# Performance work log

Measured on AMD Instinct MI355X. Metric: run time of the kernel, lower is better.

The kernel has to match this reference:

```python
import jax, jax.numpy as jnp
import numpy as np

B, T, N, F_IN = 8, 16, 1000, 16
E = 16000
H, D = 4, 32          # heads, gat_hidden_shape
HL = 64               # lstm hidden
OUT = 8
NEG_SLOPE = 0.2       # PyG GATConv default


def setup_inputs() -> dict:
    key = jax.random.key(0)
    ks = jax.random.split(key, 10)
    def init(k, shape, fan):
        return (jax.random.normal(k, shape, jnp.float32) / np.sqrt(fan)).astype(jnp.float32)
    x = jax.random.normal(ks[0], (B, T, N, F_IN), jnp.float32)
    edge_index = jax.random.randint(ks[1], (2, E), 0, N)
    W_gat = init(ks[2], (F_IN, H * D), F_IN)       # GATConv lin weight
    att_src = init(ks[3], (H, D), D)
    att_dst = init(ks[4], (H, D), D)
    b_gat = jnp.zeros((H * D,), jnp.float32)
    W_ih = init(ks[5], (4 * HL, H * D), H * D)     # LSTM, gate order i,f,g,o
    W_hh = init(ks[6], (4 * HL, HL), HL)
    b_ih = jnp.zeros((4 * HL,), jnp.float32)
    b_hh = jnp.zeros((4 * HL,), jnp.float32)
    W_clf = init(ks[7], (OUT, HL), HL)
    b_clf = jnp.zeros((OUT,), jnp.float32)
    return {"x": x, "edge_index": edge_index, "W_gat": W_gat, "att_src": att_src,
            "att_dst": att_dst, "b_gat": b_gat, "W_ih": W_ih, "W_hh": W_hh,
            "b_ih": b_ih, "b_hh": b_hh, "W_clf": W_clf, "b_clf": b_clf}


def reference(x, edge_index, W_gat, att_src, att_dst, b_gat,
              W_ih, W_hh, b_ih, b_hh, W_clf, b_clf):
    Bx, Tx, Nx, Fx = x.shape
    x_flat = x.reshape(Bx * Tx, Nx, Fx)
    # PyG GATConv adds self-loops by default
    loop = jnp.arange(Nx)
    src = jnp.concatenate([edge_index[0], loop])
    dst = jnp.concatenate([edge_index[1], loop])

    def gat_graph(xg):  # xg: [N, F]
        xp = (xg @ W_gat).reshape(Nx, H, D)                 # [N,H,D]
        a_s = jnp.einsum('nhd,hd->nh', xp, att_src)         # [N,H]
        a_d = jnp.einsum('nhd,hd->nh', xp, att_dst)
        e = jax.nn.leaky_relu(a_s[src] + a_d[dst], NEG_SLOPE)  # [E+N,H]
        m = jax.ops.segment_max(e, dst, num_segments=Nx)       # per-target softmax
        ex = jnp.exp(e - m[dst])
        denom = jax.ops.segment_sum(ex, dst, num_segments=Nx)
        alpha = ex / denom[dst]                                # [E+N,H]
        out = jax.ops.segment_sum(alpha[..., None] * xp[src], dst, num_segments=Nx)
        return out.reshape(Nx, H * D) + b_gat                  # [N, H*D]

    gat = jax.vmap(gat_graph)(x_flat)          # [B*T, N, H*D]
    gat = jax.nn.relu(gat)
    pooled = gat.max(axis=1)                   # global_max_pool -> [B*T, H*D]
    seq = pooled.reshape(Bx, Tx, H * D)

    h0 = jnp.zeros((Bx, HL), jnp.float32)
    c0 = jnp.zeros((Bx, HL), jnp.float32)

    def step(carry, xt):  # xt: [B, H*D]
        h, c = carry
        gates = xt @ W_ih.T + h @ W_hh.T + b_ih + b_hh
        i, f, g, o = jnp.split(gates, 4, axis=-1)
        i, f, o = jax.nn.sigmoid(i), jax.nn.sigmoid(f), jax.nn.sigmoid(o)
        g = jnp.tanh(g)
        c = f * c + i * g
        h = o * jnp.tanh(c)
        return (h, c), None

    (hT, _), _ = jax.lax.scan(step, (h0, c0), seq.transpose(1, 0, 2))
    return hT @ W_clf.T + b_clf                # [B, OUT]
```

## Files before the change

kernel.cpp:

```cpp
#include <hip/hip_runtime.h>
#include <hip/hip_bf16.h>
#include <stdint.h>

namespace {
constexpr int kB = 8, kT = 16, kN = 1000, kF = 16;
constexpr int kE = 16000;
constexpr int kH = 4, kHD = 128;
constexpr int kHL = 64, kOUT = 8;
constexpr int kG = kB * kT;
constexpr float kNeg = 0.2f;
constexpr int kNB = 25;
constexpr int kNPB = 40;
constexpr int kPre = 1024;
constexpr int kNPW = 32;
constexpr int kBCAP = 64;

constexpr size_t CX_WG   = 0;
constexpr size_t CX_ATS  = CX_WG   + 2048;
constexpr size_t CX_ATD  = CX_ATS  + 128;
constexpr size_t CX_BG   = CX_ATD  + 128;
constexpr size_t CX_WIH  = CX_BG   + 128;
constexpr size_t CX_WHH  = CX_WIH  + 32768;
constexpr size_t CX_BIH  = CX_WHH  + 16384;
constexpr size_t CX_BHH  = CX_BIH  + 256;
constexpr size_t CX_WCLF = CX_BHH  + 256;
constexpr size_t CX_BCLF = CX_WCLF + 512;
constexpr size_t CX_TOTAL = CX_BCLF + 8;

constexpr size_t OFF_FLAG  = 0;
constexpr size_t OFF_ROW   = 256;
constexpr size_t OFF_COL   = 4352;
constexpr size_t OFF_POOL  = 68608;
constexpr size_t OFF_CANON = 134400;
constexpr size_t OFF_AS    = 239872;
constexpr size_t OFF_PPART = OFF_AS + (size_t)kG * 288000;
constexpr size_t PPART_BYTES = (size_t)kG * kNB * kHD * 4;
constexpr size_t OFF_BUCKET = OFF_PPART + PPART_BYTES;
constexpr size_t BUCKET_BYTES = (size_t)kN * kBCAP * 4;

constexpr int kSetupBlocks = 41;
}

typedef float v2f __attribute__((ext_vector_type(2)));

__device__ __forceinline__ float bf2f(unsigned short u) {
    return __uint_as_float(((uint32_t)u) << 16);
}
__device__ __forceinline__ float blo(uint32_t u) { return __uint_as_float(u << 16); }
__device__ __forceinline__ float bhi(uint32_t u) { return __uint_as_float(u & 0xffff0000u); }
__device__ __forceinline__ unsigned short f2bf(float f) {
    uint32_t u = __float_as_uint(f);
    uint32_t r = (u + 0x7fff + ((u >> 16) & 1)) >> 16;
    return (unsigned short)r;
}
__device__ __forceinline__ float sigm(float x) { return 1.f / (1.f + __expf(-x)); }

__device__ __forceinline__ int detect_isf_wave(const unsigned short* xs, int lane) {
    const uint2 s4 = *(const uint2*)(xs + lane * 4);
    const unsigned short u0 = (unsigned short)(s4.x & 0xffff);
    const unsigned short u1 = (unsigned short)(s4.x >> 16);
    const unsigned short u2 = (unsigned short)(s4.y & 0xffff);
    const unsigned short u3 = (unsigned short)(s4.y >> 16);
    int loc = 0;
#define ISF_TEST(u) { int ex = ((u) >> 7) & 0xff; \
    loc += ((u) == 0 || (ex >= 97 && ex <= 143)) ? 1 : 0; }
    ISF_TEST(u0) ISF_TEST(u1) ISF_TEST(u2) ISF_TEST(u3)
#undef ISF_TEST
#pragma unroll
    for (int sft = 1; sft < 64; sft <<= 1) loc += __shfl_xor(loc, sft, 64);
    return (loc >= 205) ? 0 : 1;
}

struct ConvArgs {
    const unsigned short* src[10];
    int n[10];
};

__global__ __launch_bounds__(256) void mega_setup(
        const void* __restrict__ xraw, const int* __restrict__ ei,
        ConvArgs ca,
        const unsigned short* __restrict__ WgR,
        const unsigned short* __restrict__ atsR,
        const unsigned short* __restrict__ atdR,
        int* __restrict__ flag, int* __restrict__ rowdeg, int* __restrict__ col,
        int* __restrict__ bucket, int use_bucket,
        unsigned short* __restrict__ canon,
        unsigned short* __restrict__ xp_all,
        float* __restrict__ as_all, float* __restrict__ ad_all,
        unsigned int* __restrict__ pooled) {
    const int t = threadIdx.x;
    const unsigned short* xs = (const unsigned short*)xraw;

    if (blockIdx.x < 8) {
        const int isf = detect_isf_wave(xs, t & 63);
        if (blockIdx.x == 0 && t == 0) *flag = isf;
        const int gid = (int)blockIdx.x * 256 + t;
        size_t base = 0;
        for (int s = 0; s < 10; ++s) {
            const int n = ca.n[s];
            if (isf) {
                const float* fp = (const float*)ca.src[s];
                for (int i = gid; i < n; i += 2048) canon[base + i] = f2bf(fp[i]);
            } else {
                const unsigned short* sp = ca.src[s];
                for (int i = gid; i < n; i += 2048) canon[base + i] = sp[i];
            }
            base += (size_t)n;
        }
    } else if (blockIdx.x == 8) {
        for (int i = t; i < kG * kHD; i += 256) pooled[i] = 0u;
    } else if (blockIdx.x < kSetupBlocks) {
        if (use_bucket) {
            const int gid = (int)(blockIdx.x - 9) * 256 + t;
            const int* srcp = ei;
            const int* dstp = ei + kE;
            for (int e = gid; e < kE; e += 32 * 256) {
                const int d = dstp[e];
                const int pos = atomicAdd(&rowdeg[d], 1);
                if (pos < kBCAP) bucket[d * kBCAP + pos] = srcp[e];
            }
        } else if (blockIdx.x == 9) {
            __shared__ int cnt[1024];
            __shared__ int wtot[4];
            const int lane = t & 63, w = t >> 6;
            for (int i = t; i < 1024; i += 256) cnt[i] = 0;
            __syncthreads();
            const int* dst = ei + kE;
            for (int e = t; e < kE; e += 256) atomicAdd(&cnt[dst[e]], 1);
            __syncthreads();
            const int n0 = 4 * t;
            int c0 = cnt[n0], c1 = cnt[n0 + 1], c2 = cnt[n0 + 2], c3 = cnt[n0 + 3];
            int s0 = c0, s1 = s0 + c1, s2 = s1 + c2, s3 = s2 + c3;
            int tot = s3;
#pragma unroll
            for (int sft = 1; sft < 64; sft <<= 1) {
                int v = __shfl_up(tot, sft, 64);
                if (lane >= sft) tot += v;
            }
            if (lane == 63) wtot[w] = tot;
            __syncthreads();
            int wexcl = 0;
            for (int j = 0; j < w; ++j) wexcl += wtot[j];
            const int excl = wexcl + tot - s3;
            if (t == 0) rowdeg[0] = 0;
            if (n0 < kN) {
                rowdeg[n0 + 1] = excl + s0;
                rowdeg[n0 + 2] = excl + s1;
                rowdeg[n0 + 3] = excl + s2;
                rowdeg[n0 + 4] = excl + s3;
            }
            __syncthreads();
            cnt[n0] = excl; cnt[n0 + 1] = excl + s0;
            cnt[n0 + 2] = excl + s1; cnt[n0 + 3] = excl + s2;
            __syncthreads();
            for (int e = t; e < kE; e += 256) {
                int d0 = dst[e];
                int pos = atomicAdd(&cnt[d0], 1);
                col[pos] = ei[e];
            }
        }
    } else {
        const int lane = t & 63;
        const int isf = detect_isf_wave(xs, lane);
        const int wv = t >> 6;
        const int wid = (int)(blockIdx.x - kSetupBlocks) * 4 + wv;

        float wA[kF], wB[kF];
        float as0, as1, ad0, ad1;
        if (isf) {
            const float* wf = (const float*)WgR;
#pragma unroll
            for (int f = 0; f < kF; ++f) {
                const float2 wp = ((const float2*)(wf + (size_t)f * kHD))[lane];
                wA[f] = wp.x; wB[f] = wp.y;
            }
            const float2 sv = ((const float2*)atsR)[lane];
            as0 = sv.x; as1 = sv.y;
            const float2 dv2 = ((const float2*)atdR)[lane];
            ad0 = dv2.x; ad1 = dv2.y;
        } else {
            const uint32_t* w32 = (const uint32_t*)WgR;
#pragma unroll
            for (int f = 0; f < kF; ++f) {
                const uint32_t u = w32[f * 64 + lane];
                wA[f] = blo(u); wB[f] = bhi(u);
            }
            const uint32_t us = ((const uint32_t*)atsR)[lane];
            as0 = blo(us); as1 = bhi(us);
            const uint32_t ud = ((const uint32_t*)atdR)[lane];
            ad0 = blo(ud); ad1 = bhi(ud);
        }

        uint32_t* xp32 = (uint32_t*)xp_all;
        const int nStart = wid * kNPW;
        const int nEnd = min(nStart + kNPW, kG * kN);
        if (nStart >= nEnd) return;

        auto emit = [&](int node, const float* xv) {
            float vA = 0.f, vB = 0.f;
#pragma unroll
            for (int f = 0; f < kF; ++f) {
                vA = fmaf(xv[f], wA[f], vA);
                vB = fmaf(xv[f], wB[f], vB);
            }
            xp32[(size_t)node * 64 + lane] =
                (uint32_t)f2bf(vA) | ((uint32_t)f2bf(vB) << 16);
            float aS = vA * as0 + vB * as1;
            float aD = vA * ad0 + vB * ad1;
#pragma unroll
            for (int sft = 1; sft < 16; sft <<= 1) {
                aS += __shfl_xor(aS, sft, 64);
                aD += __shfl_xor(aD, sft, 64);
            }
            if ((lane & 15) == 0) {
                as_all[(size_t)node * kH + (lane >> 4)] = aS;
                ad_all[(size_t)node * kH + (lane >> 4)] = aD;
            }
        };

        if (isf) {
            const float4* xr = (const float4*)xraw;
            float4 c0 = xr[(size_t)nStart * 4 + 0], c1 = xr[(size_t)nStart * 4 + 1];
            float4 c2 = xr[(size_t)nStart * 4 + 2], c3 = xr[(size_t)nStart * 4 + 3];
            for (int node = nStart; node < nEnd; ++node) {
                const int nn = (node + 1 < nEnd) ? node + 1 : node;
                const float4 p0 = xr[(size_t)nn * 4 + 0];
                const float4 p1 = xr[(size_t)nn * 4 + 1];
                const float4 p2 = xr[(size_t)nn * 4 + 2];
                const float4 p3 = xr[(size_t)nn * 4 + 3];
                const float xv[kF] = {c0.x, c0.y, c0.z, c0.w, c1.x, c1.y, c1.z, c1.w,
                                      c2.x, c2.y, c2.z, c2.w, c3.x, c3.y, c3.z, c3.w};
                emit(node, xv);
                c0 = p0; c1 = p1; c2 = p2; c3 = p3;
            }
        } else {
            const uint4* xr = (const uint4*)xs;
            uint4 c0 = xr[(size_t)nStart * 2 + 0], c1 = xr[(size_t)nStart * 2 + 1];
            for (int node = nStart; node < nEnd; ++node) {
                const int nn = (node + 1 < nEnd) ? node + 1 : node;
                const uint4 p0 = xr[(size_t)nn * 2 + 0];
                const uint4 p1 = xr[(size_t)nn * 2 + 1];
                const float xv[kF] = {
                    blo(c0.x), bhi(c0.x), blo(c0.y), bhi(c0.y),
                    blo(c0.z), bhi(c0.z), blo(c0.w), bhi(c0.w),
                    blo(c1.x), bhi(c1.x), blo(c1.y), bhi(c1.y),
                    blo(c1.z), bhi(c1.z), blo(c1.w), bhi(c1.w)};
                emit(node, xv);
                c0 = p0; c1 = p1;
            }
        }
    }
}

__global__ __launch_bounds__(256) void gat_aggregate(
        const int* __restrict__ rowdeg, const int* __restrict__ col,
        const int* __restrict__ bucket, int use_bucket,
        const unsigned short* __restrict__ xp,
        const float* __restrict__ a_s, const float* __restrict__ a_d,
        const unsigned short* __restrict__ bg,
        unsigned int* __restrict__ pooled,
        float* __restrict__ part, int use_part) {
    __shared__ float2 colal[4][4][68];
    __shared__ float pm[4][kHD];

    const int w = threadIdx.x >> 6;
    const int lane = threadIdx.x & 63;
    const int sub = lane >> 4;
    const int cl = lane & 15;
    const int hh = cl >> 2;
    const int xcd = blockIdx.x & 7;
    const int j = blockIdx.x >> 3;
    const int gl = xcd + 8 * (j / kNB);
    const int blk = j % kNB;
    const size_t gn = (size_t)gl * kN;
    const char* xpcl = (const char*)(xp + gn * kHD) + cl * 16;
    const float4* as4 = (const float4*)a_s + gn;
    const float4* ad4 = (const float4*)a_d + gn;
    const uint32_t* bg32 = (const uint32_t*)bg;
    float bgv[8];
#pragma unroll
    for (int jb = 0; jb < 4; ++jb) {
        uint32_t u = bg32[cl * 4 + jb];
        bgv[2 * jb] = blo(u);
        bgv[2 * jb + 1] = bhi(u);
    }
    float pool[8];
#pragma unroll
    for (int jb = 0; jb < 8; ++jb) pool[jb] = 0.f;

    auto pairBody = [&](v2f* acc2, float& dh, int e0) {
        const float2 cA = colal[w][hh][e0 + sub];
        const float2 cB = colal[w][hh][e0 + 4 + sub];
        const uint4 uA = *(const uint4*)(xpcl + __float_as_int(cA.x));
        const uint4 uB = *(const uint4*)(xpcl + __float_as_int(cB.x));
        const float aA = cA.y, aB = cB.y;
        const v2f aA2 = {aA, aA}, aB2 = {aB, aB};
        acc2[0] += aA2 * (v2f){blo(uA.x), bhi(uA.x)};
        acc2[1] += aA2 * (v2f){blo(uA.y), bhi(uA.y)};
        acc2[2] += aA2 * (v2f){blo(uA.z), bhi(uA.z)};
        acc2[3] += aA2 * (v2f){blo(uA.w), bhi(uA.w)};
        acc2[0] += aB2 * (v2f){blo(uB.x), bhi(uB.x)};
        acc2[1] += aB2 * (v2f){blo(uB.y), bhi(uB.y)};
        acc2[2] += aB2 * (v2f){blo(uB.z), bhi(uB.z)};
        acc2[3] += aB2 * (v2f){blo(uB.w), bhi(uB.w)};
        dh += aA + aB;
    };
    auto singleBody = [&](v2f* acc2, float& dh, int e0) {
        const float2 cA = colal[w][hh][e0 + sub];
        const uint4 uA = *(const uint4*)(xpcl + __float_as_int(cA.x));
        const float aA = cA.y;
        const v2f aA2 = {aA, aA};
        acc2[0] += aA2 * (v2f){blo(uA.x), bhi(uA.x)};
        acc2[1] += aA2 * (v2f){blo(uA.y), bhi(uA.y)};
        acc2[2] += aA2 * (v2f){blo(uA.z), bhi(uA.z)};
        acc2[3] += aA2 * (v2f){blo(uA.w), bhi(uA.w)};
        dh += aA;
    };
    auto finishNode = [&](v2f* acc2, float dh) {
        float acc[8];
#pragma unroll
        for (int jb = 0; jb < 4; ++jb) {
            acc[2 * jb] = acc2[jb].x;
            acc[2 * jb + 1] = acc2[jb].y;
        }
#pragma unroll
        for (int jb = 0; jb < 8; ++jb) {
            acc[jb] += __shfl_xor(acc[jb], 16, 64);
            acc[jb] += __shfl_xor(acc[jb], 32, 64);
        }
        dh += __shfl_xor(dh, 16, 64);
        dh += __shfl_xor(dh, 32, 64);
        const float inv = 1.f / dh;
#pragma unroll
        for (int jb = 0; jb < 8; ++jb) {
            const float o = acc[jb] * inv + bgv[jb];
            pool[jb] = fmaxf(pool[jb], o > 0.f ? o : 0.f);
        }
    };

    if (use_bucket) {
        int nidx = blk * kNPB + w;
        int degc = min(rowdeg[nidx], 63);
        int sc = (lane < degc) ? bucket[nidx * kBCAP + lane] : nidx;
        float4 avc = as4[sc];
        float4 dvc = ad4[nidx];

        for (int it = 0; it < 10; ++it) {
            const int deg = degc;
            const int E = deg + 1;
            const int cntP = (E + 3) & ~3;
            const int s = sc;
            const float4 av = avc;
            const float4 dv = dvc;

            if (lane < cntP) {
                float p0 = 0.f, p1 = 0.f, p2 = 0.f, p3 = 0.f;
                if (lane < E) {
                    float t0 = av.x + dv.x, t1 = av.y + dv.y;
                    float t2 = av.z + dv.z, t3 = av.w + dv.w;
                    t0 = t0 > 0.f ? t0 : kNeg * t0;
                    t1 = t1 > 0.f ? t1 : kNeg * t1;
                    t2 = t2 > 0.f ? t2 : kNeg * t2;
                    t3 = t3 > 0.f ? t3 : kNeg * t3;
                    p0 = __expf(t0); p1 = __expf(t1);
                    p2 = __expf(t2); p3 = __expf(t3);
                }
                const float cf = __int_as_float(s << 8);
                colal[w][0][lane] = make_float2(cf, p0);
                colal[w][1][lane] = make_float2(cf, p1);
                colal[w][2][lane] = make_float2(cf, p2);
                colal[w][3][lane] = make_float2(cf, p3);
            }

            const int itn = (it + 1 == 10) ? 0 : (it + 1);
            const int n_nxt = blk * kNPB + itn * 4 + w;
            degc = min(rowdeg[n_nxt], 63);
            dvc = ad4[n_nxt];
            sc = (lane < degc) ? bucket[n_nxt * kBCAP + lane] : n_nxt;
            nidx = n_nxt;

            v2f acc2[4];
#pragma unroll
            for (int jb = 0; jb < 4; ++jb) acc2[jb] = (v2f){0.f, 0.f};
            float dh = 0.f;
            int e0 = 0;
            if (cntP >= 8) { pairBody(acc2, dh, 0); e0 = 8; }
            avc = as4[sc];
            for (; e0 + 8 <= cntP; e0 += 8) pairBody(acc2, dh, e0);
            if (e0 < cntP) singleBody(acc2, dh, e0);

            finishNode(acc2, dh);
        }
    } else {
        for (int it = 0; it < 10; ++it) {
            const int n = blk * kNPB + it * 4 + w;
            const int r0 = rowdeg[n];
            const int deg = rowdeg[n + 1] - r0;
            const int E = deg + 1;
            const float4 dv = ad4[n];
            v2f acc2[4];
#pragma unroll
            for (int jb = 0; jb < 4; ++jb) acc2[jb] = (v2f){0.f, 0.f};
            float dh = 0.f;

            for (int base = 0; base < E; base += 64) {
                const int cnt = min(64, E - base);
                const int cntP = (cnt + 3) & ~3;
                if (lane < cntP) {
                    const int eg = base + lane;
                    const bool act = lane < cnt;
                    const int s = (act && eg < deg) ? col[r0 + eg] : n;
                    float p0 = 0.f, p1 = 0.f, p2 = 0.f, p3 = 0.f;
                    if (act) {
                        const float4 av = as4[s];
                        float t0 = av.x + dv.x, t1 = av.y + dv.y;
                        float t2 = av.z + dv.z, t3 = av.w + dv.w;
                        t0 = t0 > 0.f ? t0 : kNeg * t0;
                        t1 = t1 > 0.f ? t1 : kNeg * t1;
                        t2 = t2 > 0.f ? t2 : kNeg * t2;
                        t3 = t3 > 0.f ? t3 : kNeg * t3;
                        p0 = __expf(t0); p1 = __expf(t1);
                        p2 = __expf(t2); p3 = __expf(t3);
                    }
                    const float cf = __int_as_float(s << 8);
                    colal[w][0][lane] = make_float2(cf, p0);
                    colal[w][1][lane] = make_float2(cf, p1);
                    colal[w][2][lane] = make_float2(cf, p2);
                    colal[w][3][lane] = make_float2(cf, p3);
                }
                int e0 = 0;
                for (; e0 + 8 <= cntP; e0 += 8) pairBody(acc2, dh, e0);
                if (e0 < cntP) singleBody(acc2, dh, e0);
            }
            finishNode(acc2, dh);
        }
    }

    if (sub == 0) {
#pragma unroll
        for (int jb = 0; jb < 8; ++jb) pm[w][cl * 8 + jb] = pool[jb];
    }
    __syncthreads();
    if (w == 0 && sub == 0) {
        if (use_part) {
            float* dst = part + ((size_t)gl * kNB + blk) * kHD;
#pragma unroll
            for (int jb = 0; jb < 8; ++jb) {
                const int c = cl * 8 + jb;
                dst[c] = fmaxf(fmaxf(pm[0][c], pm[1][c]), fmaxf(pm[2][c], pm[3][c]));
            }
        } else {
            const size_t gp = (size_t)gl * kHD;
#pragma unroll
            for (int jb = 0; jb < 8; ++jb) {
                const int c = cl * 8 + jb;
                float vmax = fmaxf(fmaxf(pm[0][c], pm[1][c]), fmaxf(pm[2][c], pm[3][c]));
                atomicMax(pooled + gp + c, __float_as_uint(vmax));
            }
        }
    }
}

__global__ __launch_bounds__(256) void lstm_head(
        const float* __restrict__ pooled, const float* __restrict__ part,
        int use_part,
        const unsigned short* __restrict__ Wih,
        const unsigned short* __restrict__ Whh,
        const unsigned short* __restrict__ bih,
        const unsigned short* __restrict__ bhh,
        const unsigned short* __restrict__ Wclf,
        const unsigned short* __restrict__ bclf,
        const int* __restrict__ flag,
        void* __restrict__ out) {
    const int b = blockIdx.x;
    const int r = threadIdx.x;
    __shared__ float xt[kHD];
    __shared__ float hs[kHL];
    __shared__ float gates[4 * kHL];

    uint32_t wih[64];
    const uint32_t* pw = (const uint32_t*)(Wih + (size_t)r * kHD);
#pragma unroll
    for (int j = 0; j < 64; ++j) wih[j] = pw[j];
    uint32_t whh[32];
    const uint32_t* ph = (const uint32_t*)(Whh + (size_t)r * kHL);
#pragma unroll
    for (int j = 0; j < 32; ++j) whh[j] = ph[j];
    const float bias = bf2f(bih[r]) + bf2f(bhh[r]);

    float c_st = 0.f;
    if (r < kHL) hs[r] = 0.f;
    __syncthreads();

    for (int t = 0; t < kT; ++t) {
        const size_t g = (size_t)b * kT + t;
        if (r < kHD) {
            if (use_part) {
                const float* ps = part + g * kNB * kHD + r;
                float v = ps[0];
#pragma unroll
                for (int k = 1; k < kNB; ++k) v = fmaxf(v, ps[(size_t)k * kHD]);
                xt[r] = v;
            } else {
                xt[r] = pooled[g * kHD + r];
            }
        }
        __syncthreads();
        float a0 = 0.f, a1 = 0.f, a2 = 0.f, a3 = 0.f;
#pragma unroll
        for (int j = 0; j < 64; j += 4) {
            uint32_t u0 = wih[j], u1 = wih[j + 1], u2 = wih[j + 2], u3 = wih[j + 3];
            a0 += blo(u0) * xt[2 * j + 0] + bhi(u0) * xt[2 * j + 1];
            a1 += blo(u1) * xt[2 * j + 2] + bhi(u1) * xt[2 * j + 3];
            a2 += blo(u2) * xt[2 * j + 4] + bhi(u2) * xt[2 * j + 5];
            a3 += blo(u3) * xt[2 * j + 6] + bhi(u3) * xt[2 * j + 7];
        }
#pragma unroll
        for (int j = 0; j < 32; j += 4) {
            uint32_t u0 = whh[j], u1 = whh[j + 1], u2 = whh[j + 2], u3 = whh[j + 3];
            a0 += blo(u0) * hs[2 * j + 0] + bhi(u0) * hs[2 * j + 1];
            a1 += blo(u1) * hs[2 * j + 2] + bhi(u1) * hs[2 * j + 3];
            a2 += blo(u2) * hs[2 * j + 4] + bhi(u2) * hs[2 * j + 5];
            a3 += blo(u3) * hs[2 * j + 6] + bhi(u3) * hs[2 * j + 7];
        }
        gates[r] = bias + (a0 + a1) + (a2 + a3);
        __syncthreads();
        if (r < kHL) {
            const float iv = sigm(gates[r]);
            const float fv = sigm(gates[kHL + r]);
            const float gv = tanhf(gates[2 * kHL + r]);
            const float ov = sigm(gates[3 * kHL + r]);
            c_st = fv * c_st + iv * gv;
            hs[r] = ov * tanhf(c_st);
        }
        __syncthreads();
    }
    if (r < kOUT) {
        float acc = bf2f(bclf[r]);
#pragma unroll
        for (int k = 0; k < kHL; ++k) acc += hs[k] * bf2f(Wclf[r * kHL + k]);
        if (*flag) ((float*)out)[b * kOUT + r] = acc;
        else ((__hip_bfloat16*)out)[b * kOUT + r] = __float2bfloat16(acc);
    }
}

extern "C" void kernel_launch(void* const* d_in, const int* in_sizes, int n_in,
                              void* d_out, int out_size, void* d_ws, size_t ws_size,
                              hipStream_t stream) {
    const int* ei = (const int*)d_in[1];

    char* ws = (char*)d_ws;
    int*            flag   = (int*)(ws + OFF_FLAG);
    int*            rowdeg = (int*)(ws + OFF_ROW);
    int*            colv   = (int*)(ws + OFF_COL);
    unsigned int*   pooled = (unsigned int*)(ws + OFF_POOL);
    unsigned short* canon  = (unsigned short*)(ws + OFF_CANON);

    unsigned short* cBg   = canon + CX_BG;
    unsigned short* cWih  = canon + CX_WIH;
    unsigned short* cWhh  = canon + CX_WHH;
    unsigned short* cBih  = canon + CX_BIH;
    unsigned short* cBhh  = canon + CX_BHH;
    unsigned short* cWclf = canon + CX_WCLF;
    unsigned short* cBclf = canon + CX_BCLF;

    float*          a_s = (float*)(ws + OFF_AS);
    float*          a_d = (float*)(ws + OFF_AS + (size_t)kG * 16000);
    unsigned short* xp  = (unsigned short*)(ws + OFF_AS + (size_t)kG * 32000);

    const int use_part   = (ws_size >= OFF_PPART + PPART_BYTES) ? 1 : 0;
    const int use_bucket = (ws_size >= OFF_BUCKET + BUCKET_BYTES) ? 1 : 0;
    float* part   = (float*)(ws + OFF_PPART);
    int*   bucket = (int*)(ws + OFF_BUCKET);

    ConvArgs ca;
    const int sizes[10] = {2048, 128, 128, 128, 32768, 16384, 256, 256, 512, 8};
    const int which[10] = {2, 3, 4, 5, 6, 7, 8, 9, 10, 11};
    for (int i = 0; i < 10; ++i) {
        ca.src[i] = (const unsigned short*)d_in[which[i]];
        ca.n[i] = sizes[i];
    }

    hipMemsetAsync(ws + OFF_ROW, 0, 4096, stream);

    mega_setup<<<kSetupBlocks + kPre, 256, 0, stream>>>(
        d_in[0], ei, ca,
        (const unsigned short*)d_in[2], (const unsigned short*)d_in[3],
        (const unsigned short*)d_in[4],
        flag, rowdeg, colv, bucket, use_bucket, canon, xp, a_s, a_d, pooled);
    gat_aggregate<<<kG * kNB, 256, 0, stream>>>(rowdeg, colv, bucket, use_bucket,
                                                xp, a_s, a_d, cBg,
                                                pooled, part, use_part);
    lstm_head<<<kB, 256, 0, stream>>>((const float*)pooled, part, use_part,
                                      cWih, cWhh, cBih, cBhh,
                                      cWclf, cBclf, flag, d_out);
}
```

Baseline: 199.3 us.

## Halve nodes per aggregation block and pool via atomicMax instead of partial buffers

```diff
diff --git a/kernel.cpp b/kernel.cpp
--- a/kernel.cpp
+++ b/kernel.cpp
@@ -9,8 +9,9 @@
 constexpr int kHL = 64, kOUT = 8;
 constexpr int kG = kB * kT;
 constexpr float kNeg = 0.2f;
-constexpr int kNB = 25;
-constexpr int kNPB = 40;
+constexpr int kNB = 50;
+constexpr int kNPB = 20;
+constexpr int kIters = 5;
 constexpr int kPre = 1024;
 constexpr int kNPW = 32;
 constexpr int kBCAP = 64;
@@ -33,9 +34,7 @@
 constexpr size_t OFF_POOL  = 68608;
 constexpr size_t OFF_CANON = 134400;
 constexpr size_t OFF_AS    = 239872;
-constexpr size_t OFF_PPART = OFF_AS + (size_t)kG * 288000;
-constexpr size_t PPART_BYTES = (size_t)kG * kNB * kHD * 4;
-constexpr size_t OFF_BUCKET = OFF_PPART + PPART_BYTES;
+constexpr size_t OFF_BUCKET = OFF_AS + (size_t)kG * 288000;
 constexpr size_t BUCKET_BYTES = (size_t)kN * kBCAP * 4;
 
 constexpr int kSetupBlocks = 41;
@@ -258,8 +257,7 @@
         const unsigned short* __restrict__ xp,
         const float* __restrict__ a_s, const float* __restrict__ a_d,
         const unsigned short* __restrict__ bg,
-        unsigned int* __restrict__ pooled,
-        float* __restrict__ part, int use_part) {
+        unsigned int* __restrict__ pooled) {
     __shared__ float2 colal[4][4][68];
     __shared__ float pm[4][kHD];
 
@@ -339,13 +337,13 @@
     };
 
     if (use_bucket) {
-        int nidx = blk * kNPB + w;
-        int degc = min(rowdeg[nidx], 63);
-        int sc = (lane < degc) ? bucket[nidx * kBCAP + lane] : nidx;
+        int n0i = blk * kNPB + w;
+        int degc = min(rowdeg[n0i], 63);
+        int sc = (lane < degc) ? bucket[n0i * kBCAP + lane] : n0i;
         float4 avc = as4[sc];
-        float4 dvc = ad4[nidx];
-
-        for (int it = 0; it < 10; ++it) {
+        float4 dvc = ad4[n0i];
+
+        for (int it = 0; it < kIters; ++it) {
             const int deg = degc;
             const int E = deg + 1;
             const int cntP = (E + 3) & ~3;
@@ -372,12 +370,11 @@
                 colal[w][3][lane] = make_float2(cf, p3);
             }
 
-            const int itn = (it + 1 == 10) ? 0 : (it + 1);
+            const int itn = (it + 1 == kIters) ? 0 : (it + 1);
             const int n_nxt = blk * kNPB + itn * 4 + w;
             degc = min(rowdeg[n_nxt], 63);
             dvc = ad4[n_nxt];
             sc = (lane < degc) ? bucket[n_nxt * kBCAP + lane] : n_nxt;
-            nidx = n_nxt;
 
             v2f acc2[4];
 #pragma unroll
@@ -392,7 +389,7 @@
             finishNode(acc2, dh);
         }
     } else {
-        for (int it = 0; it < 10; ++it) {
+        for (int it = 0; it < kIters; ++it) {
             const int n = blk * kNPB + it * 4 + w;
             const int r0 = rowdeg[n];
             const int deg = rowdeg[n + 1] - r0;
@@ -442,28 +439,18 @@
     }
     __syncthreads();
     if (w == 0 && sub == 0) {
-        if (use_part) {
-            float* dst = part + ((size_t)gl * kNB + blk) * kHD;
-#pragma unroll
-            for (int jb = 0; jb < 8; ++jb) {
-                const int c = cl * 8 + jb;
-                dst[c] = fmaxf(fmaxf(pm[0][c], pm[1][c]), fmaxf(pm[2][c], pm[3][c]));
-            }
-        } else {
-            const size_t gp = (size_t)gl * kHD;
-#pragma unroll
-            for (int jb = 0; jb < 8; ++jb) {
-                const int c = cl * 8 + jb;
-                float vmax = fmaxf(fmaxf(pm[0][c], pm[1][c]), fmaxf(pm[2][c], pm[3][c]));
-                atomicMax(pooled + gp + c, __float_as_uint(vmax));
-            }
+        const size_t gp = (size_t)gl * kHD;
+#pragma unroll
+        for (int jb = 0; jb < 8; ++jb) {
+            const int c = cl * 8 + jb;
+            float vmax = fmaxf(fmaxf(pm[0][c], pm[1][c]), fmaxf(pm[2][c], pm[3][c]));
+            atomicMax(pooled + gp + c, __float_as_uint(vmax));
         }
     }
 }
 
 __global__ __launch_bounds__(256) void lstm_head(
-        const float* __restrict__ pooled, const float* __restrict__ part,
-        int use_part,
+        const float* __restrict__ pooled,
         const unsigned short* __restrict__ Wih,
         const unsigned short* __restrict__ Whh,
         const unsigned short* __restrict__ bih,
@@ -494,17 +481,7 @@
 
     for (int t = 0; t < kT; ++t) {
         const size_t g = (size_t)b * kT + t;
-        if (r < kHD) {
-            if (use_part) {
-                const float* ps = part + g * kNB * kHD + r;
-                float v = ps[0];
-#pragma unroll
-                for (int k = 1; k < kNB; ++k) v = fmaxf(v, ps[(size_t)k * kHD]);
-                xt[r] = v;
-            } else {
-                xt[r] = pooled[g * kHD + r];
-            }
-        }
+        if (r < kHD) xt[r] = pooled[g * kHD + r];
         __syncthreads();
         float a0 = 0.f, a1 = 0.f, a2 = 0.f, a3 = 0.f;
 #pragma unroll
@@ -568,10 +545,8 @@
     float*          a_d = (float*)(ws + OFF_AS + (size_t)kG * 16000);
     unsigned short* xp  = (unsigned short*)(ws + OFF_AS + (size_t)kG * 32000);
 
-    const int use_part   = (ws_size >= OFF_PPART + PPART_BYTES) ? 1 : 0;
     const int use_bucket = (ws_size >= OFF_BUCKET + BUCKET_BYTES) ? 1 : 0;
-    float* part   = (float*)(ws + OFF_PPART);
-    int*   bucket = (int*)(ws + OFF_BUCKET);
+    int* bucket = (int*)(ws + OFF_BUCKET);
 
     ConvArgs ca;
     const int sizes[10] = {2048, 128, 128, 128, 32768, 16384, 256, 256, 512, 8};
@@ -589,9 +564,8 @@
         (const unsigned short*)d_in[4],
         flag, rowdeg, colv, bucket, use_bucket, canon, xp, a_s, a_d, pooled);
     gat_aggregate<<<kG * kNB, 256, 0, stream>>>(rowdeg, colv, bucket, use_bucket,
-                                                xp, a_s, a_d, cBg,
-                                                pooled, part, use_part);
-    lstm_head<<<kB, 256, 0, stream>>>((const float*)pooled, part, use_part,
+                                                xp, a_s, a_d, cBg, pooled);
+    lstm_head<<<kB, 256, 0, stream>>>((const float*)pooled,
                                       cWih, cWhh, cBih, cBhh,
                                       cWclf, cBclf, flag, d_out);
 }
```

Result: slower. 239.0 us (+19.9%).
